# Performance work log

Measured on AMD Instinct MI355X. Metric: run time of the kernel, lower is better.

Reference implementation:

```python
import jax, jax.numpy as jnp
import numpy as np

N, E, F_IN = 50000, 800000, 128
H, C, CLS, G = 8, 32, 16, 64
NEG_SLOPE = 0.2


def setup_inputs() -> dict:
    key = jax.random.key(0)
    ks = jax.random.split(key, 11)
    s = 0.05
    return {
        "x": jax.random.normal(ks[0], (N, F_IN), jnp.float32),
        "edge_index": jax.random.randint(ks[1], (2, E), 0, N, jnp.int32),
        "batch": jnp.sort(jax.random.randint(ks[2], (N,), 0, G, jnp.int32)),
        "W1": jax.random.normal(ks[3], (F_IN, H * C), jnp.float32) * s,
        "a1_src": jax.random.normal(ks[4], (H, C), jnp.float32) * s,
        "a1_dst": jax.random.normal(ks[5], (H, C), jnp.float32) * s,
        "b1": jax.random.normal(ks[6], (H * C,), jnp.float32) * s,
        "W2": jax.random.normal(ks[7], (H * C, CLS), jnp.float32) * s,
        "a2_src": jax.random.normal(ks[8], (1, CLS), jnp.float32) * s,
        "a2_dst": jax.random.normal(ks[9], (1, CLS), jnp.float32) * s,
        "b2": jax.random.normal(ks[10], (CLS,), jnp.float32) * s,
    }


def _gat_conv(x, src, dst, W, a_s, a_d, b, concat):
    n = x.shape[0]
    Hh, Cc = a_s.shape
    xp = (x @ W).reshape(n, Hh, Cc)                      # [N,H,C]
    al_s = jnp.einsum("nhc,hc->nh", xp, a_s)             # [N,H]
    al_d = jnp.einsum("nhc,hc->nh", xp, a_d)
    e = jax.nn.leaky_relu(al_s[src] + al_d[dst], NEG_SLOPE)  # [E,H]
    m = jax.ops.segment_max(e, dst, num_segments=n)      # segment softmax over dst
    ex = jnp.exp(e - m[dst])
    denom = jax.ops.segment_sum(ex, dst, num_segments=n)
    alpha = ex / denom[dst]                              # [E,H]
    out = jax.ops.segment_sum(xp[src] * alpha[:, :, None], dst, num_segments=n)
    out = out.reshape(n, Hh * Cc) if concat else out.mean(axis=1)
    return out + b


def reference(x, edge_index, batch, W1, a1_src, a1_dst, b1, W2, a2_src, a2_dst, b2):
    n = x.shape[0]
    loops = jnp.arange(n, dtype=edge_index.dtype)        # PyG add_self_loops=True
    ei = jnp.concatenate([edge_index, jnp.stack([loops, loops])], axis=1)
    src, dst = ei[0], ei[1]
    h = jax.nn.elu(_gat_conv(x, src, dst, W1, a1_src, a1_dst, b1, True))
    h = _gat_conv(h, src, dst, W2, a2_src, a2_dst, b2, False)
    counts = jax.ops.segment_sum(jnp.ones((n,), h.dtype), batch, num_segments=G)
    pooled = jax.ops.segment_sum(h, batch, num_segments=G) / jnp.maximum(counts, 1.0)[:, None]
    return jax.nn.log_softmax(pooled, axis=1)
```

## Files before the change

kernel.cpp:

```cpp
#include <hip/hip_runtime.h>
#include <math.h>

#define N_NODES 50000
#define N_EDGES 800000
#define FDIM 128
#define NH 8
#define NC 32
#define D1 256
#define NCLS 16
#define NGRP 64
#define NEG 0.2f
#define E_TOT (N_EDGES + N_NODES)
#define NB_N 196
#define G1_BLOCKS 782
#define E_CHUNK 4096
#define NCHUNK 196
#define NBIN 196

typedef __attribute__((ext_vector_type(4))) unsigned short u16x4;
typedef __attribute__((ext_vector_type(8))) short short8;
typedef __attribute__((ext_vector_type(4))) float f32x4;

static __device__ __forceinline__ float bf2f(unsigned short u) {
    return __uint_as_float(((unsigned int)u) << 16);
}
static __device__ __forceinline__ unsigned short f2bf(float f) {
    unsigned int b = __float_as_uint(f);
    return (unsigned short)((b + 0x7FFFu + ((b >> 16) & 1u)) >> 16);
}

__global__ __launch_bounds__(256) void k_init(
    const float* __restrict__ W1, unsigned short* __restrict__ w1p,
    float* __restrict__ poolS, float* __restrict__ poolC,
    const int* __restrict__ ei, int* __restrict__ binmat) {
    __shared__ int h[NBIN];
    int c = blockIdx.x;
    for (int b = threadIdx.x; b < NBIN; b += 256) h[b] = 0;
    __syncthreads();
    int e0 = c * E_CHUNK;
    int e1 = e0 + E_CHUNK; if (e1 > N_EDGES) e1 = N_EDGES;
    for (int e = e0 + threadIdx.x; e < e1; e += 256)
        atomicAdd(&h[ei[N_EDGES + e] >> 8], 1);
    int i = blockIdx.x * 256 + threadIdx.x;
    if (i < NGRP * NCLS) poolS[i] = 0.f;
    if (i < NGRP) poolC[i] = 0.f;
    if (i < FDIM * D1) {
        int ks = i >> 13;
        int r = i & 8191;
        int nt2 = r >> 9;
        int r2 = r & 511;
        int lane = r2 >> 3, e = r2 & 7;
        int k = ks * 32 + (lane >> 4) * 8 + e;
        int col = nt2 * 16 + (lane & 15);
        w1p[i] = f2bf(W1[k * D1 + col]);
    }
    __syncthreads();
    for (int b = threadIdx.x; b < NBIN; b += 256) binmat[b * NCHUNK + c] = h[b];
}

__global__ __launch_bounds__(256) void k_binprescan(int* __restrict__ binmat,
                                                    int* __restrict__ binTot) {
    __shared__ int sh[256];
    int b = blockIdx.x, t = threadIdx.x;
    int v = (t < NCHUNK) ? binmat[b * NCHUNK + t] : 0;
    sh[t] = v;
    __syncthreads();
    for (int d = 1; d < 256; d <<= 1) {
        int tv = (t >= d) ? sh[t - d] : 0;
        __syncthreads();
        sh[t] += tv;
        __syncthreads();
    }
    if (t < NCHUNK) binmat[b * NCHUNK + t] = sh[t] - v;
    if (t == 255) binTot[b] = sh[255];
}

__global__ __launch_bounds__(256) void k_gemm1m(
    const float* __restrict__ x, const unsigned short* __restrict__ w1p,
    const float* __restrict__ a1s, const float* __restrict__ a1d,
    unsigned short* __restrict__ xp1b, float* __restrict__ al1s,
    float* __restrict__ al1d) {
    const int l = threadIdx.x & 63;
    const int wid = threadIdx.x >> 6;
    const int wr = wid >> 1, wc = wid & 1;
    const int l15 = l & 15, l4 = l >> 4;
    const int base = blockIdx.x * 64;
    const int r0 = base + wr * 32;

    f32x4 acc[2][8] = {};
#pragma unroll
    for (int ks = 0; ks < 4; ++ks) {
        const int kk = ks * 32 + l4 * 8;
        short8 af[2];
#pragma unroll
        for (int rt = 0; rt < 2; ++rt) {
            int row = r0 + rt * 16 + l15;
            float4 v0 = make_float4(0.f, 0.f, 0.f, 0.f), v1 = v0;
            if (row < N_NODES) {
                const float* xr = x + (size_t)row * FDIM + kk;
                v0 = *(const float4*)xr;
                v1 = *(const float4*)(xr + 4);
            }
            short8 a;
            a[0] = (short)f2bf(v0.x); a[1] = (short)f2bf(v0.y);
            a[2] = (short)f2bf(v0.z); a[3] = (short)f2bf(v0.w);
            a[4] = (short)f2bf(v1.x); a[5] = (short)f2bf(v1.y);
            a[6] = (short)f2bf(v1.z); a[7] = (short)f2bf(v1.w);
            af[rt] = a;
        }
#pragma unroll
        for (int nt = 0; nt < 8; ++nt) {
            int nt2 = wc * 8 + nt;
            short8 bf_ = *(const short8*)&w1p[(size_t)((ks * 16 + nt2) * 64 + l) * 8];
            acc[0][nt] = __builtin_amdgcn_mfma_f32_16x16x32_bf16(af[0], bf_, acc[0][nt], 0, 0, 0);
            acc[1][nt] = __builtin_amdgcn_mfma_f32_16x16x32_bf16(af[1], bf_, acc[1][nt], 0, 0, 0);
        }
    }
#pragma unroll
    for (int rt = 0; rt < 2; ++rt) {
        int rbase = r0 + rt * 16 + l4 * 4;
#pragma unroll
        for (int nt = 0; nt < 8; ++nt) {
            int col = wc * 128 + nt * 16 + l15;
            f32x4 c = acc[rt][nt];
#pragma unroll
            for (int r = 0; r < 4; ++r) {
                int row = rbase + r;
                if (row < N_NODES) xp1b[(size_t)row * D1 + col] = f2bf(c[r]);
            }
        }
    }
#pragma unroll
    for (int hl = 0; hl < 4; ++hl) {
        int hg = wc * 4 + hl;
        float as0 = a1s[hg * NC + l15], as1 = a1s[hg * NC + 16 + l15];
        float ad0 = a1d[hg * NC + l15], ad1 = a1d[hg * NC + 16 + l15];
#pragma unroll
        for (int rt = 0; rt < 2; ++rt) {
            f32x4 c0 = acc[rt][2 * hl], c1 = acc[rt][2 * hl + 1];
#pragma unroll
            for (int r = 0; r < 4; ++r) {
                float ss = c0[r] * as0 + c1[r] * as1;
                float dd = c0[r] * ad0 + c1[r] * ad1;
#pragma unroll
                for (int msk = 1; msk < 16; msk <<= 1) {
                    ss += __shfl_xor(ss, msk);
                    dd += __shfl_xor(dd, msk);
                }
                int row = r0 + rt * 16 + l4 * 4 + r;
                if (l15 == 0 && row < N_NODES) {
                    al1s[row * NH + hg] = ss;
                    al1d[row * NH + hg] = dd;
                }
            }
        }
    }
}

__global__ __launch_bounds__(256) void k_binscatter(const int* __restrict__ ei,
                                                    const int* __restrict__ offs,
                                                    const int* __restrict__ binTot,
                                                    int* __restrict__ binned) {
    __shared__ int cur[NBIN];
    __shared__ int sb[256];
    int c = blockIdx.x;
    int t = threadIdx.x;
    int v = (t < NBIN) ? binTot[t] : 0;
    sb[t] = v;
    __syncthreads();
    for (int d = 1; d < 256; d <<= 1) {
        int tv = (t >= d) ? sb[t - d] : 0;
        __syncthreads();
        sb[t] += tv;
        __syncthreads();
    }
    if (t < NBIN) cur[t] = (sb[t] - v) + offs[t * NCHUNK + c];
    __syncthreads();
    int e0 = c * E_CHUNK;
    int e1 = e0 + E_CHUNK; if (e1 > N_EDGES) e1 = N_EDGES;
    for (int e = e0 + t; e < e1; e += 256) {
        int s = ei[e], d = ei[N_EDGES + e];
        int pos = atomicAdd(&cur[d >> 8], 1);
        binned[pos] = s | ((d & 255) << 16);
    }
}

__global__ __launch_bounds__(256) void k_bincsr(const int* __restrict__ binTot,
                                                const int* __restrict__ binned,
                                                int* __restrict__ rowptr,
                                                int* __restrict__ cnt,
                                                int* __restrict__ esrc) {
    __shared__ int sh[256];
    __shared__ int lcnt[256];
    __shared__ int lcur[256];
    int b = blockIdx.x;
    int t = threadIdx.x;
    int v = (t < NBIN) ? binTot[t] : 0;
    sh[t] = v;
    __syncthreads();
    for (int d = 1; d < 256; d <<= 1) {
        int tv = (t >= d) ? sh[t - d] : 0;
        __syncthreads();
        sh[t] += tv;
        __syncthreads();
    }
    int estart = (b == 0) ? 0 : sh[b - 1];
    int eend = sh[b];
    __syncthreads();
    int nbase = b * 256;
    int nin = N_NODES - nbase; if (nin > 256) nin = 256;
    lcnt[t] = 0;
    __syncthreads();
    for (int e = estart + t; e < eend; e += 256)
        atomicAdd(&lcnt[(binned[e] >> 16) & 255], 1);
    __syncthreads();
    int myc = lcnt[t] + (t < nin ? 1 : 0);
    sh[t] = myc;
    __syncthreads();
    for (int d = 1; d < 256; d <<= 1) {
        int tv = (t >= d) ? sh[t - d] : 0;
        __syncthreads();
        sh[t] += tv;
        __syncthreads();
    }
    int excl = sh[t] - myc;
    int outbase = estart + nbase;
    int rp = outbase + excl;
    if (t < nin) {
        rowptr[nbase + t] = rp;
        cnt[nbase + t] = myc;
        esrc[rp] = nbase + t;
    }
    lcur[t] = rp + (t < nin ? 1 : 0);
    __syncthreads();
    for (int e = estart + t; e < eend; e += 256) {
        int vv = binned[e];
        int pos = atomicAdd(&lcur[(vv >> 16) & 255], 1);
        esrc[pos] = vv & 0xFFFF;
    }
}

__global__ __launch_bounds__(256) void k_att1f(
    const unsigned short* __restrict__ xp1b, const float* __restrict__ al1s,
    const float* __restrict__ al1d, const float* __restrict__ b1,
    const float* __restrict__ W2, const float* __restrict__ a2s,
    const float* __restrict__ a2d, const int* __restrict__ rowptr,
    const int* __restrict__ cnt, const int* __restrict__ esrc,
    float* __restrict__ xp2, float* __restrict__ al2s, float* __restrict__ al2d) {
    __shared__ int s_src[4][64];
    __shared__ float s_alpha[4][64 * 8];
    int wv = threadIdx.x >> 6;
    int lane = threadIdx.x & 63;
    int n = blockIdx.x * 4 + wv;
    int start = rowptr[n];
    int deg = cnt[n];
    int dcap = deg < 64 ? deg : 64;
    int dpad = (dcap + 7) & ~7;
    for (int j = lane; j < dpad; j += 64)
        s_src[wv][j] = (j < dcap) ? esrc[start + j] : n;
    int npad = (dpad - dcap) * 8;
    if (lane < npad) s_alpha[wv][dcap * 8 + lane] = 0.f;
    int h = lane & 7, eg = lane >> 3;
    float ald = al1d[n * NH + h];
    float m = -1e30f;
    for (int j = eg; j < dcap; j += 8) {
        int s = s_src[wv][j];
        float v = al1s[s * NH + h] + ald;
        v = fmaxf(v, NEG * v);
        s_alpha[wv][j * 8 + h] = v;
        m = fmaxf(m, v);
    }
    if (deg > 64) {
        for (int j = 64 + eg; j < deg; j += 8) {
            int s = esrc[start + j];
            float v = al1s[s * NH + h] + ald;
            m = fmaxf(m, fmaxf(v, NEG * v));
        }
    }
    for (int msk = 8; msk < 64; msk <<= 1) m = fmaxf(m, __shfl_xor(m, msk));
    float den = 0.f;
    for (int j = eg; j < dcap; j += 8) {
        float e = __expf(s_alpha[wv][j * 8 + h] - m);
        s_alpha[wv][j * 8 + h] = e;
        den += e;
    }
    if (deg > 64) {
        for (int j = 64 + eg; j < deg; j += 8) {
            int s = esrc[start + j];
            float v = al1s[s * NH + h] + ald;
            v = fmaxf(v, NEG * v);
            den += __expf(v - m);
        }
    }
    for (int msk = 8; msk < 64; msk <<= 1) den += __shfl_xor(den, msk);
    int hh = lane >> 3;
    int cbb = lane << 3;
    float rd2 = 1.f / __shfl(den, hh);
    float m2 = __shfl(m, hh);
    float a0 = 0.f, a1 = 0.f, a2 = 0.f, a3 = 0.f;
    for (int j0 = 0; j0 < dpad; j0 += 8) {
        int off[8];
        float aw[8];
#pragma unroll
        for (int k = 0; k < 8; ++k) {
            int s = s_src[wv][j0 + k];
            aw[k] = s_alpha[wv][(j0 + k) * 8 + hh];
            off[k] = (s << 9) + cbb;
        }
#pragma unroll
        for (int k = 0; k < 8; ++k) {
            u16x4 xv = *(const u16x4*)((const char*)xp1b + off[k]);
            a0 = fmaf(aw[k], bf2f(xv[0]), a0);
            a1 = fmaf(aw[k], bf2f(xv[1]), a1);
            a2 = fmaf(aw[k], bf2f(xv[2]), a2);
            a3 = fmaf(aw[k], bf2f(xv[3]), a3);
        }
    }
    if (deg > 64) {
        float ald2 = al1d[n * NH + hh];
        for (int j = 64; j < deg; ++j) {
            int s = esrc[start + j];
            float v = al1s[s * NH + hh] + ald2;
            v = fmaxf(v, NEG * v);
            float al = __expf(v - m2);
            u16x4 xv = *(const u16x4*)((const char*)xp1b + (s << 9) + cbb);
            a0 = fmaf(al, bf2f(xv[0]), a0);
            a1 = fmaf(al, bf2f(xv[1]), a1);
            a2 = fmaf(al, bf2f(xv[2]), a2);
            a3 = fmaf(al, bf2f(xv[3]), a3);
        }
    }
    float* h_l = &s_alpha[wv][0];
    int cb = lane << 2;
    float4 bb = *(const float4*)(b1 + cb);
    a0 = fmaf(a0, rd2, bb.x);
    a1 = fmaf(a1, rd2, bb.y);
    a2 = fmaf(a2, rd2, bb.z);
    a3 = fmaf(a3, rd2, bb.w);
    a0 = a0 > 0.f ? a0 : expm1f(a0);
    a1 = a1 > 0.f ? a1 : expm1f(a1);
    a2 = a2 > 0.f ? a2 : expm1f(a2);
    a3 = a3 > 0.f ? a3 : expm1f(a3);
    *(float4*)&h_l[cb] = make_float4(a0, a1, a2, a3);
    {
        int o = lane & 15, q = lane >> 4;
        const float* hq = h_l + q * 4;
        const float* wq = W2 + q * 64 + o;
        float po0 = 0.f, po1 = 0.f, po2 = 0.f, po3 = 0.f;
#pragma unroll
        for (int cc = 0; cc < 16; ++cc) {
            float4 hv = *(const float4*)(hq + cc * 16);
            const float* w = wq + cc * 256;
            po0 = fmaf(hv.x, w[0],  po0);
            po1 = fmaf(hv.y, w[16], po1);
            po2 = fmaf(hv.z, w[32], po2);
            po3 = fmaf(hv.w, w[48], po3);
        }
        float po = (po0 + po1) + (po2 + po3);
        po += __shfl_xor(po, 16);
        po += __shfl_xor(po, 32);
        float ts = po * a2s[o];
        float td = po * a2d[o];
#pragma unroll
        for (int msk = 1; msk < 16; msk <<= 1) {
            ts += __shfl_xor(ts, msk);
            td += __shfl_xor(td, msk);
        }
        if (lane < 16) xp2[(size_t)n * NCLS + lane] = po;
        if (lane == 0) { al2s[n] = ts; al2d[n] = td; }
    }
}

__global__ __launch_bounds__(256) void k_att2(
    const float* __restrict__ xp2, const float* __restrict__ al2s,
    const float* __restrict__ al2d, const float* __restrict__ b2,
    const int* __restrict__ rowptr, const int* __restrict__ cnt,
    const int* __restrict__ esrc, float* __restrict__ out2) {
    __shared__ int s_src[4][64];
    __shared__ float s_a[4][64];
    int wave = threadIdx.x >> 6;
    int lane = threadIdx.x & 63;
    int n = blockIdx.x * 4 + wave;
    int start = rowptr[n];
    int deg = cnt[n];
    int dcap = deg < 64 ? deg : 64;
    int dpad = (dcap + 7) & ~7;
    for (int j = lane; j < dpad; j += 64)
        s_src[wave][j] = (j < dcap) ? esrc[start + j] : n;
    if (lane < dpad - dcap) s_a[wave][dcap + lane] = 0.f;
    float ald = al2d[n];
    float m = -1e30f;
    for (int j = lane; j < dcap; j += 64) {
        int s = s_src[wave][j];
        float v = al2s[s] + ald;
        v = fmaxf(v, NEG * v);
        s_a[wave][j] = v;
        m = fmaxf(m, v);
    }
    if (deg > 64) {
        for (int j = 64 + lane; j < deg; j += 64) {
            float v = al2s[esrc[start + j]] + ald;
            m = fmaxf(m, fmaxf(v, NEG * v));
        }
    }
    for (int msk = 1; msk < 64; msk <<= 1) m = fmaxf(m, __shfl_xor(m, msk));
    float den = 0.f;
    for (int j = lane; j < dcap; j += 64) {
        float e = __expf(s_a[wave][j] - m);
        s_a[wave][j] = e;
        den += e;
    }
    if (deg > 64) {
        for (int j = 64 + lane; j < deg; j += 64) {
            float v = al2s[esrc[start + j]] + ald;
            v = fmaxf(v, NEG * v);
            den += __expf(v - m);
        }
    }
    for (int msk = 1; msk < 64; msk <<= 1) den += __shfl_xor(den, msk);
    float rden = 1.f / den;
    int c = lane & 15;
    int eg = lane >> 4;
    float acc = 0.f;
    for (int j0 = 0; j0 < dpad; j0 += 8) {
#pragma unroll
        for (int k = 0; k < 2; ++k) {
            int e = j0 + eg + 4 * k;
            float aw = s_a[wave][e];
            int s = s_src[wave][e];
            acc = fmaf(aw, xp2[(size_t)s * NCLS + c], acc);
        }
    }
    if (deg > 64) {
        for (int j = 64 + eg; j < deg; j += 4) {
            int s = esrc[start + j];
            float v = al2s[s] + ald;
            v = fmaxf(v, NEG * v);
            acc += __expf(v - m) * xp2[(size_t)s * NCLS + c];
        }
    }
    acc += __shfl_xor(acc, 16);
    acc += __shfl_xor(acc, 32);
    if (lane < 16) out2[(size_t)n * NCLS + lane] = acc * rden + b2[lane];
}

__global__ __launch_bounds__(256) void k_pool(
    const float* __restrict__ out2, const int* __restrict__ batch,
    float* __restrict__ poolS, float* __restrict__ poolC) {
    __shared__ float sacc[NGRP * NCLS];
    __shared__ float scnt[NGRP];
    for (int i = threadIdx.x; i < NGRP * NCLS; i += 256) sacc[i] = 0.f;
    if (threadIdx.x < NGRP) scnt[threadIdx.x] = 0.f;
    __syncthreads();
    int n = blockIdx.x * 256 + threadIdx.x;
    if (n < N_NODES) {
        int g = batch[n];
        atomicAdd(&scnt[g], 1.f);
#pragma unroll
        for (int q = 0; q < 4; ++q) {
            float4 v = *(const float4*)(out2 + (size_t)n * NCLS + q * 4);
            atomicAdd(&sacc[g * NCLS + q * 4 + 0], v.x);
            atomicAdd(&sacc[g * NCLS + q * 4 + 1], v.y);
            atomicAdd(&sacc[g * NCLS + q * 4 + 2], v.z);
            atomicAdd(&sacc[g * NCLS + q * 4 + 3], v.w);
        }
    }
    __syncthreads();
    for (int i = threadIdx.x; i < NGRP * NCLS; i += 256)
        if (sacc[i] != 0.f) atomicAdd(&poolS[i], sacc[i]);
    if (threadIdx.x < NGRP && scnt[threadIdx.x] != 0.f)
        atomicAdd(&poolC[threadIdx.x], scnt[threadIdx.x]);
}

__global__ void k_final(const float* __restrict__ poolS,
                        const float* __restrict__ poolC, float* __restrict__ out) {
    int g = threadIdx.x;
    if (g >= NGRP) return;
    float inv = 1.f / fmaxf(poolC[g], 1.f);
    float v[NCLS];
    float m = -1e30f;
#pragma unroll
    for (int c = 0; c < NCLS; ++c) {
        v[c] = poolS[g * NCLS + c] * inv;
        m = fmaxf(m, v[c]);
    }
    float s = 0.f;
#pragma unroll
    for (int c = 0; c < NCLS; ++c) s += expf(v[c] - m);
    float lse = m + logf(s);
#pragma unroll
    for (int c = 0; c < NCLS; ++c) out[g * NCLS + c] = v[c] - lse;
}

extern "C" void kernel_launch(void* const* d_in, const int* in_sizes, int n_in,
                              void* d_out, int out_size, void* d_ws, size_t ws_size,
                              hipStream_t stream) {
    const float* x    = (const float*)d_in[0];
    const int*   ei   = (const int*)d_in[1];
    const int*   batch = (const int*)d_in[2];
    const float* W1   = (const float*)d_in[3];
    const float* a1s  = (const float*)d_in[4];
    const float* a1d  = (const float*)d_in[5];
    const float* b1   = (const float*)d_in[6];
    const float* W2   = (const float*)d_in[7];
    const float* a2s  = (const float*)d_in[8];
    const float* a2d  = (const float*)d_in[9];
    const float* b2   = (const float*)d_in[10];
    float* out = (float*)d_out;

    float* f = (float*)d_ws;
    float* al1s_ = f;  f += (size_t)N_NODES * NH;
    float* al1d_ = f;  f += (size_t)N_NODES * NH;
    float* xp2   = f;  f += (size_t)N_NODES * NCLS;
    float* al2s_ = f;  f += N_NODES;
    float* al2d_ = f;  f += N_NODES;
    float* out2  = f;  f += (size_t)N_NODES * NCLS;
    float* poolS = f;  f += NGRP * NCLS;
    float* poolC = f;  f += NGRP;
    unsigned short* xp1b = (unsigned short*)f;
    unsigned short* w1p  = xp1b + (size_t)N_NODES * D1;
    int* binmat  = (int*)(w1p + FDIM * D1);
    int* binTot  = binmat + NBIN * NCHUNK;
    int* binned  = binTot + NBIN;
    int* rowptr  = binned + N_EDGES;
    int* cnt     = rowptr + N_NODES;
    int* esrc    = cnt + N_NODES;

    k_init<<<NB_N, 256, 0, stream>>>(W1, w1p, poolS, poolC, ei, binmat);
    k_binprescan<<<NBIN, 256, 0, stream>>>(binmat, binTot);
    k_gemm1m<<<G1_BLOCKS, 256, 0, stream>>>(x, w1p, a1s, a1d, xp1b, al1s_, al1d_);
    k_binscatter<<<NCHUNK, 256, 0, stream>>>(ei, binmat, binTot, binned);
    k_bincsr<<<NBIN, 256, 0, stream>>>(binTot, binned, rowptr, cnt, esrc);
    k_att1f<<<N_NODES / 4, 256, 0, stream>>>(xp1b, al1s_, al1d_, b1, W2, a2s, a2d,
                                             rowptr, cnt, esrc, xp2, al2s_, al2d_);
    k_att2<<<N_NODES / 4, 256, 0, stream>>>(xp2, al2s_, al2d_, b2, rowptr, cnt, esrc, out2);
    k_pool<<<NB_N, 256, 0, stream>>>(out2, batch, poolS, poolC);
    k_final<<<1, 64, 0, stream>>>(poolS, poolC, out);
}
```

Measured before the change: 187.4 us.

## Fuse mean pooling into layer-2 attention and transpose W2 for vector loads

Fuses the pooling step into the layer-2 attention kernel. Each block accumulates its four nodes' outputs into shared-memory group sums and flushes them with global atomics, which removes the out2 buffer and one kernel launch. Separately, W2 is transposed once in the init kernel so the layer-1 epilogue can read the weights as float4. The trade-off is that each att2 block now zeroes and scans a 1024-entry shared array for only four nodes, adding per-block overhead and many more global atomic flushes (12500 blocks instead of 196).

```diff
diff --git a/kernel.cpp b/kernel.cpp
--- a/kernel.cpp
+++ b/kernel.cpp
@@ -30,7 +30,8 @@
 }
 
 __global__ __launch_bounds__(256) void k_init(
-    const float* __restrict__ W1, unsigned short* __restrict__ w1p,
+    const float* __restrict__ W1, const float* __restrict__ W2,
+    unsigned short* __restrict__ w1p, float* __restrict__ w2t,
     float* __restrict__ poolS, float* __restrict__ poolC,
     const int* __restrict__ ei, int* __restrict__ binmat) {
     __shared__ int h[NBIN];
@@ -44,6 +45,10 @@
     int i = blockIdx.x * 256 + threadIdx.x;
     if (i < NGRP * NCLS) poolS[i] = 0.f;
     if (i < NGRP) poolC[i] = 0.f;
+    if (i < NCLS * D1) {
+        int o = i >> 8, cc = i & 255;
+        w2t[i] = W2[cc * NCLS + o];
+    }
     if (i < FDIM * D1) {
         int ks = i >> 13;
         int r = i & 8191;
@@ -243,7 +248,7 @@
 __global__ __launch_bounds__(256) void k_att1f(
     const unsigned short* __restrict__ xp1b, const float* __restrict__ al1s,
     const float* __restrict__ al1d, const float* __restrict__ b1,
-    const float* __restrict__ W2, const float* __restrict__ a2s,
+    const float* __restrict__ w2t, const float* __restrict__ a2s,
     const float* __restrict__ a2d, const int* __restrict__ rowptr,
     const int* __restrict__ cnt, const int* __restrict__ esrc,
     float* __restrict__ xp2, float* __restrict__ al2s, float* __restrict__ al2d) {
@@ -345,16 +350,16 @@
     {
         int o = lane & 15, q = lane >> 4;
         const float* hq = h_l + q * 4;
-        const float* wq = W2 + q * 64 + o;
+        const float* wq = w2t + o * 256 + q * 4;
         float po0 = 0.f, po1 = 0.f, po2 = 0.f, po3 = 0.f;
 #pragma unroll
         for (int cc = 0; cc < 16; ++cc) {
             float4 hv = *(const float4*)(hq + cc * 16);
-            const float* w = wq + cc * 256;
-            po0 = fmaf(hv.x, w[0],  po0);
-            po1 = fmaf(hv.y, w[16], po1);
-            po2 = fmaf(hv.z, w[32], po2);
-            po3 = fmaf(hv.w, w[48], po3);
+            float4 wvv = *(const float4*)(wq + cc * 16);
+            po0 = fmaf(hv.x, wvv.x, po0);
+            po1 = fmaf(hv.y, wvv.y, po1);
+            po2 = fmaf(hv.z, wvv.z, po2);
+            po3 = fmaf(hv.w, wvv.w, po3);
         }
         float po = (po0 + po1) + (po2 + po3);
         po += __shfl_xor(po, 16);
@@ -371,16 +376,22 @@
     }
 }
 
-__global__ __launch_bounds__(256) void k_att2(
+__global__ __launch_bounds__(256) void k_att2p(
     const float* __restrict__ xp2, const float* __restrict__ al2s,
     const float* __restrict__ al2d, const float* __restrict__ b2,
     const int* __restrict__ rowptr, const int* __restrict__ cnt,
-    const int* __restrict__ esrc, float* __restrict__ out2) {
+    const int* __restrict__ esrc, const int* __restrict__ batch,
+    float* __restrict__ poolS, float* __restrict__ poolC) {
     __shared__ int s_src[4][64];
     __shared__ float s_a[4][64];
+    __shared__ float sacc[NGRP * NCLS];
+    __shared__ float scnt[NGRP];
     int wave = threadIdx.x >> 6;
     int lane = threadIdx.x & 63;
     int n = blockIdx.x * 4 + wave;
+    for (int i = threadIdx.x; i < NGRP * NCLS; i += 256) sacc[i] = 0.f;
+    if (threadIdx.x < NGRP) scnt[threadIdx.x] = 0.f;
+    __syncthreads();
     int start = rowptr[n];
     int deg = cnt[n];
     int dcap = deg < 64 ? deg : 64;
@@ -441,30 +452,9 @@
     }
     acc += __shfl_xor(acc, 16);
     acc += __shfl_xor(acc, 32);
-    if (lane < 16) out2[(size_t)n * NCLS + lane] = acc * rden + b2[lane];
-}
-
-__global__ __launch_bounds__(256) void k_pool(
-    const float* __restrict__ out2, const int* __restrict__ batch,
-    float* __restrict__ poolS, float* __restrict__ poolC) {
-    __shared__ float sacc[NGRP * NCLS];
-    __shared__ float scnt[NGRP];
-    for (int i = threadIdx.x; i < NGRP * NCLS; i += 256) sacc[i] = 0.f;
-    if (threadIdx.x < NGRP) scnt[threadIdx.x] = 0.f;
-    __syncthreads();
-    int n = blockIdx.x * 256 + threadIdx.x;
-    if (n < N_NODES) {
-        int g = batch[n];
-        atomicAdd(&scnt[g], 1.f);
-#pragma unroll
-        for (int q = 0; q < 4; ++q) {
-            float4 v = *(const float4*)(out2 + (size_t)n * NCLS + q * 4);
-            atomicAdd(&sacc[g * NCLS + q * 4 + 0], v.x);
-            atomicAdd(&sacc[g * NCLS + q * 4 + 1], v.y);
-            atomicAdd(&sacc[g * NCLS + q * 4 + 2], v.z);
-            atomicAdd(&sacc[g * NCLS + q * 4 + 3], v.w);
-        }
-    }
+    int g = batch[n];
+    if (lane < 16) atomicAdd(&sacc[g * NCLS + lane], acc * rden + b2[lane]);
+    if (lane == 0) atomicAdd(&scnt[g], 1.f);
     __syncthreads();
     for (int i = threadIdx.x; i < NGRP * NCLS; i += 256)
         if (sacc[i] != 0.f) atomicAdd(&poolS[i], sacc[i]);
@@ -514,9 +504,9 @@
     float* xp2   = f;  f += (size_t)N_NODES * NCLS;
     float* al2s_ = f;  f += N_NODES;
     float* al2d_ = f;  f += N_NODES;
-    float* out2  = f;  f += (size_t)N_NODES * NCLS;
     float* poolS = f;  f += NGRP * NCLS;
     float* poolC = f;  f += NGRP;
+    float* w2t   = f;  f += NCLS * D1;
     unsigned short* xp1b = (unsigned short*)f;
     unsigned short* w1p  = xp1b + (size_t)N_NODES * D1;
     int* binmat  = (int*)(w1p + FDIM * D1);
@@ -526,14 +516,14 @@
     int* cnt     = rowptr + N_NODES;
     int* esrc    = cnt + N_NODES;
 
-    k_init<<<NB_N, 256, 0, stream>>>(W1, w1p, poolS, poolC, ei, binmat);
+    k_init<<<NB_N, 256, 0, stream>>>(W1, W2, w1p, w2t, poolS, poolC, ei, binmat);
     k_binprescan<<<NBIN, 256, 0, stream>>>(binmat, binTot);
     k_gemm1m<<<G1_BLOCKS, 256, 0, stream>>>(x, w1p, a1s, a1d, xp1b, al1s_, al1d_);
     k_binscatter<<<NCHUNK, 256, 0, stream>>>(ei, binmat, binTot, binned);
     k_bincsr<<<NBIN, 256, 0, stream>>>(binTot, binned, rowptr, cnt, esrc);
-    k_att1f<<<N_NODES / 4, 256, 0, stream>>>(xp1b, al1s_, al1d_, b1, W2, a2s, a2d,
+    k_att1f<<<N_NODES / 4, 256, 0, stream>>>(xp1b, al1s_, al1d_, b1, w2t, a2s, a2d,
                                              rowptr, cnt, esrc, xp2, al2s_, al2d_);
-    k_att2<<<N_NODES / 4, 256, 0, stream>>>(xp2, al2s_, al2d_, b2, rowptr, cnt, esrc, out2);
-    k_pool<<<NB_N, 256, 0, stream>>>(out2, batch, poolS, poolC);
+    k_att2p<<<N_NODES / 4, 256, 0, stream>>>(xp2, al2s_, al2d_, b2, rowptr, cnt,
+                                             esrc, batch, poolS, poolC);
     k_final<<<1, 64, 0, stream>>>(poolS, poolC, out);
 }
```

New measurement: 301.9 us. +61.1%, slower.
